# Kernel optimization log

Measured on AMD Instinct MI355X. Metric: run time of the kernel, lower is better.

## Reference

```python
import jax, jax.numpy as jnp
import numpy as np

B, LM, LX, D = 16, 1024, 1024, 768


def setup_inputs() -> dict:
    key = jax.random.key(0)
    k1, k2, k3, k4 = jax.random.split(key, 4)
    main = jax.random.normal(k1, (B, LM, D), dtype=jnp.float32)
    x = jax.random.normal(k2, (B, LX, D), dtype=jnp.float32)
    # keras 'uniform' init ~ U(-0.05, 0.05); scale to keep activations sane
    W = jax.random.uniform(k3, (D, D), dtype=jnp.float32, minval=-0.05, maxval=0.05)
    w = jax.random.uniform(k4, (2 * D, 1), dtype=jnp.float32, minval=-0.05, maxval=0.05)
    return {"main": main, "x": x, "W": W, "w": w}


def reference(main, x, W, w):
    # bilinear co-attention scores: (main @ W) . x^T -> (B, LM, LX)
    proj = jnp.einsum('bmd,de->bme', main, W)            # (B, LM, D)
    scores = jnp.einsum('bme,bne->bmn', proj, x)         # (B, LM, LX) -- no softmax in original
    A = jnp.einsum('bmn,bnd->bmd', scores, x)            # attended features (B, LM, D)
    s = main - A
    m = main * A
    outputs = jnp.concatenate([s, m], axis=-1)           # (B, LM, 2D)
    beta = jnp.einsum('bmk,k->bm', outputs, w[:, 0])     # (B, LM) -- raw, no softmax
    pooled = jnp.einsum('bm,bmk->bk', beta, outputs)     # weighted-sum pooling (B, 2D)
    return pooled
```

## Files before the change

kernel.cpp:

```cpp
#include <hip/hip_runtime.h>

constexpr int kB  = 16;
constexpr int kLM = 1024;
constexpr int kLX = 1024;
constexpr int kD  = 768;

using short8 = __attribute__((ext_vector_type(8))) short;
using f32x4  = __attribute__((ext_vector_type(4))) float;

__device__ __forceinline__ unsigned short f2bf(float f) {
    unsigned u = __float_as_uint(f);
    u = (u + 0x7FFF + ((u >> 16) & 1)) >> 16;
    return (unsigned short)u;
}
__device__ __forceinline__ float bf2f(unsigned short h) {
    return __uint_as_float(((unsigned)h) << 16);
}

__device__ __forceinline__ void gl_lds16(const unsigned short* g, unsigned short* l) {
    auto gp = (const __attribute__((address_space(1))) unsigned int*)g;
    auto lp = (__attribute__((address_space(3))) unsigned int*)l;
    __builtin_amdgcn_global_load_lds(gp, lp, 16, 0, 0);
}

__device__ __forceinline__ void writeChunk(unsigned short* dst, float4 lo, float4 hi) {
    union { short8 v; unsigned short u[8]; } o;
    o.u[0] = f2bf(lo.x); o.u[1] = f2bf(lo.y); o.u[2] = f2bf(lo.z); o.u[3] = f2bf(lo.w);
    o.u[4] = f2bf(hi.x); o.u[5] = f2bf(hi.y); o.u[6] = f2bf(hi.z); o.u[7] = f2bf(hi.w);
    *(short8*)dst = o.v;
}

__device__ __forceinline__ size_t chunk_off(int c, int K) {
    int sr = c >> 3, s = c & 7;
    int tt = s ^ (sr & 7);
    int r  = sr * 2 + (tt >> 2);
    int q  = tt & 3;
    return (size_t)r * K + q * 8;
}

__global__ __launch_bounds__(256) void transpose_cvt_kernel(
    const float* __restrict__ x, unsigned short* __restrict__ xT) {
    __shared__ float tile[64][65];
    const int b  = blockIdx.z;
    const int l0 = blockIdx.x * 64;
    const int d0 = blockIdx.y * 64;
    const int t  = threadIdx.x;
    const int tx = t & 15, ty = t >> 4;
    const float* xb = x + ((size_t)b * kLX + l0) * kD + d0;
#pragma unroll
    for (int p = 0; p < 4; ++p) {
        int r = p * 16 + ty;
        float4 v = *(const float4*)(xb + (size_t)r * kD + tx * 4);
        *(float4*)&tile[r][tx * 4] = v;
    }
    __syncthreads();
    unsigned short* xTb = xT + ((size_t)b * kD + d0) * kLX + l0;
#pragma unroll
    for (int p = 0; p < 4; ++p) {
        int dr = p * 16 + ty;
        ushort4 o;
        o.x = f2bf(tile[tx * 4 + 0][dr]);
        o.y = f2bf(tile[tx * 4 + 1][dr]);
        o.z = f2bf(tile[tx * 4 + 2][dr]);
        o.w = f2bf(tile[tx * 4 + 3][dr]);
        *(ushort4*)(xTb + (size_t)dr * kLX + tx * 4) = o;
    }
}

template <bool AFP32, bool BFP32>
__global__ __launch_bounds__(256) void gemm_nt_kernel(
    const void* __restrict__ Av, const void* __restrict__ Bv,
    unsigned short* __restrict__ C, int M, int N, int K,
    long sA, long sB, long sC) {
    __shared__ unsigned short Asm[2][128 * 32];
    __shared__ unsigned short Bsm[2][128 * 32];
    const int b  = blockIdx.z;
    const int i0 = blockIdx.x * 128;
    const int j0 = blockIdx.y * 128;
    const int t    = threadIdx.x;
    const int wave = t >> 6, lane = t & 63;
    const int wr = (wave >> 1) * 64, wc = (wave & 1) * 64;
    const int quad = lane >> 4, l15 = lane & 15;

    const unsigned short* Abh = AFP32 ? nullptr
        : (const unsigned short*)Av + (size_t)b * sA + (size_t)i0 * K;
    const unsigned short* Bbh = BFP32 ? nullptr
        : (const unsigned short*)Bv + (size_t)b * sB + (size_t)j0 * K;
    const float* Abf = AFP32
        ? (const float*)Av + (size_t)b * sA + (size_t)i0 * K : nullptr;
    const float* Bbf = BFP32
        ? (const float*)Bv + (size_t)b * sB + (size_t)j0 * K : nullptr;

    const int c0 = t, c1 = t + 256;
    const size_t off0 = chunk_off(c0, K);
    const size_t off1 = chunk_off(c1, K);

    const int sfr  = ((l15 & 1) * 4 + quad) ^ ((l15 >> 1) & 7);
    const int aOff = wr * 32 + (l15 >> 1) * 64 + sfr * 8;
    const int bOff = wc * 32 + (l15 >> 1) * 64 + sfr * 8;

    f32x4 acc[4][4];
    const f32x4 z = {0.f, 0.f, 0.f, 0.f};
#pragma unroll
    for (int i = 0; i < 4; ++i)
#pragma unroll
        for (int j = 0; j < 4; ++j) acc[i][j] = z;

    const int T = K >> 5;
    float4 pa0, pa1, pa2, pa3, pb0, pb1, pb2, pb3;

    if constexpr (AFP32) {
        writeChunk(Asm[0] + c0 * 8, *(const float4*)(Abf + off0),
                                    *(const float4*)(Abf + off0 + 4));
        writeChunk(Asm[0] + c1 * 8, *(const float4*)(Abf + off1),
                                    *(const float4*)(Abf + off1 + 4));
    } else {
        gl_lds16(Abh + off0, Asm[0] + c0 * 8);
        gl_lds16(Abh + off1, Asm[0] + c1 * 8);
    }
    if constexpr (BFP32) {
        writeChunk(Bsm[0] + c0 * 8, *(const float4*)(Bbf + off0),
                                    *(const float4*)(Bbf + off0 + 4));
        writeChunk(Bsm[0] + c1 * 8, *(const float4*)(Bbf + off1),
                                    *(const float4*)(Bbf + off1 + 4));
    } else {
        gl_lds16(Bbh + off0, Bsm[0] + c0 * 8);
        gl_lds16(Bbh + off1, Bsm[0] + c1 * 8);
    }
    if constexpr (AFP32) {
        pa0 = *(const float4*)(Abf + off0 + 32);
        pa1 = *(const float4*)(Abf + off0 + 36);
        pa2 = *(const float4*)(Abf + off1 + 32);
        pa3 = *(const float4*)(Abf + off1 + 36);
    }
    if constexpr (BFP32) {
        pb0 = *(const float4*)(Bbf + off0 + 32);
        pb1 = *(const float4*)(Bbf + off0 + 36);
        pb2 = *(const float4*)(Bbf + off1 + 32);
        pb3 = *(const float4*)(Bbf + off1 + 36);
    }

    int buf = 0;
    for (int kt = 0; kt < T; ++kt) {
        __syncthreads();
        if (kt + 1 < T) {
            const size_t k = (size_t)(kt + 1) << 5;
            if constexpr (AFP32) {
                writeChunk(Asm[buf ^ 1] + c0 * 8, pa0, pa1);
                writeChunk(Asm[buf ^ 1] + c1 * 8, pa2, pa3);
            } else {
                gl_lds16(Abh + off0 + k, Asm[buf ^ 1] + c0 * 8);
                gl_lds16(Abh + off1 + k, Asm[buf ^ 1] + c1 * 8);
            }
            if constexpr (BFP32) {
                writeChunk(Bsm[buf ^ 1] + c0 * 8, pb0, pb1);
                writeChunk(Bsm[buf ^ 1] + c1 * 8, pb2, pb3);
            } else {
                gl_lds16(Bbh + off0 + k, Bsm[buf ^ 1] + c0 * 8);
                gl_lds16(Bbh + off1 + k, Bsm[buf ^ 1] + c1 * 8);
            }
        }
        if (kt + 2 < T) {
            const size_t k2 = (size_t)(kt + 2) << 5;
            if constexpr (AFP32) {
                pa0 = *(const float4*)(Abf + off0 + k2);
                pa1 = *(const float4*)(Abf + off0 + k2 + 4);
                pa2 = *(const float4*)(Abf + off1 + k2);
                pa3 = *(const float4*)(Abf + off1 + k2 + 4);
            }
            if constexpr (BFP32) {
                pb0 = *(const float4*)(Bbf + off0 + k2);
                pb1 = *(const float4*)(Bbf + off0 + k2 + 4);
                pb2 = *(const float4*)(Bbf + off1 + k2);
                pb3 = *(const float4*)(Bbf + off1 + k2 + 4);
            }
        }
        const unsigned short* aP = Asm[buf] + aOff;
        const unsigned short* bP = Bsm[buf] + bOff;
        short8 af[4], bg[4];
#pragma unroll
        for (int i = 0; i < 4; ++i) af[i] = *(const short8*)(aP + i * 512);
#pragma unroll
        for (int j = 0; j < 4; ++j) bg[j] = *(const short8*)(bP + j * 512);
#pragma unroll
        for (int i = 0; i < 4; ++i)
#pragma unroll
            for (int j = 0; j < 4; ++j)
                acc[i][j] = __builtin_amdgcn_mfma_f32_16x16x32_bf16(
                    af[i], bg[j], acc[i][j], 0, 0, 0);
        buf ^= 1;
    }

    unsigned short* Cb = C + (size_t)b * sC + (size_t)(i0 + wr) * N + j0 + wc;
#pragma unroll
    for (int i = 0; i < 4; ++i)
#pragma unroll
        for (int j = 0; j < 4; ++j)
#pragma unroll
            for (int r = 0; r < 4; ++r)
                Cb[(size_t)(i * 16 + quad * 4 + r) * N + j * 16 + l15] =
                    f2bf(acc[i][j][r]);
}

__global__ __launch_bounds__(256) void pool_kernel(
    const float* __restrict__ mainp, const unsigned short* __restrict__ Aout,
    const float* __restrict__ w, float* __restrict__ out) {
    __shared__ float red[4][24][64];
    const int b     = blockIdx.y;
    const int chunk = blockIdx.x;
    const int t     = threadIdx.x;
    const int wave  = t >> 6, lane = t & 63;
    float w1[12], w2[12], ps[12], pm[12];
#pragma unroll
    for (int s = 0; s < 12; ++s) {
        w1[s] = w[s * 64 + lane];
        w2[s] = w[kD + s * 64 + lane];
        ps[s] = 0.f; pm[s] = 0.f;
    }
#pragma unroll
    for (int rr = 0; rr < 4; ++rr) {
        const int row = chunk * 16 + rr * 4 + wave;
        const float* mr = mainp + ((size_t)b * kLM + row) * kD;
        const unsigned short* ar = Aout + ((size_t)b * kLM + row) * kD;
        float sv[12], mv[12], acc = 0.f;
#pragma unroll
        for (int s = 0; s < 12; ++s) {
            float m_ = mr[s * 64 + lane];
            float a_ = bf2f(ar[s * 64 + lane]);
            sv[s] = m_ - a_;
            mv[s] = m_ * a_;
            acc += sv[s] * w1[s] + mv[s] * w2[s];
        }
#pragma unroll
        for (int off = 32; off; off >>= 1) acc += __shfl_xor(acc, off);
#pragma unroll
        for (int s = 0; s < 12; ++s) { ps[s] += acc * sv[s]; pm[s] += acc * mv[s]; }
    }
#pragma unroll
    for (int s = 0; s < 12; ++s) {
        red[wave][s][lane]      = ps[s];
        red[wave][12 + s][lane] = pm[s];
    }
    __syncthreads();
    float* ob = out + (size_t)b * 2 * kD;
    for (int v = t; v < 24 * 64; v += 256) {
        const int sl = v >> 6, ln = v & 63;
        const float sum = red[0][sl][ln] + red[1][sl][ln] +
                          red[2][sl][ln] + red[3][sl][ln];
        const int d = (sl < 12) ? sl * 64 + ln : kD + (sl - 12) * 64 + ln;
        atomicAdd(&ob[d], sum);
    }
}

extern "C" void kernel_launch(void* const* d_in, const int* in_sizes, int n_in,
                              void* d_out, int out_size, void* d_ws, size_t ws_size,
                              hipStream_t stream) {
    const float* mainp = (const float*)d_in[0];
    const float* x     = (const float*)d_in[1];
    const float* W     = (const float*)d_in[2];
    const float* w     = (const float*)d_in[3];
    float* out = (float*)d_out;

    char* p = (char*)d_ws;
    unsigned short* xT = (unsigned short*)p; p += (size_t)kB * kD * kLX * 2;
    unsigned short* G  = (unsigned short*)p; p += (size_t)kB * kD * kD * 2;
    unsigned short* Mt = (unsigned short*)p; p += (size_t)kB * kD * kD * 2;
    unsigned short* Ao = (unsigned short*)p; p += (size_t)kB * kLM * kD * 2;

    hipMemsetAsync(out, 0, (size_t)kB * 2 * kD * sizeof(float), stream);

    transpose_cvt_kernel<<<dim3(kLX / 64, kD / 64, kB), 256, 0, stream>>>(x, xT);

    gemm_nt_kernel<false, false><<<dim3(kD / 128, kD / 128, kB), 256, 0, stream>>>(
        xT, xT, G, kD, kD, kLX, (long)kD * kLX, (long)kD * kLX, (long)kD * kD);
    gemm_nt_kernel<false, true><<<dim3(kD / 128, kD / 128, kB), 256, 0, stream>>>(
        G, W, Mt, kD, kD, kD, (long)kD * kD, 0L, (long)kD * kD);
    gemm_nt_kernel<true, false><<<dim3(kLM / 128, kD / 128, kB), 256, 0, stream>>>(
        mainp, Mt, Ao, kLM, kD, kD, (long)kLM * kD, (long)kD * kD, (long)kLM * kD);

    pool_kernel<<<dim3(kLM / 16, kB), 256, 0, stream>>>(mainp, Ao, w, out);
}
```

Baseline: 244.3 us.

## Triple-buffer GEMM loads, exploit Gram symmetry, pre-convert inputs, remap blocks per XCD

Several changes go in together. The GEMM is reworked into a three-stage LDS pipeline that uses async global-to-LDS loads with explicit vmcnt waits and raised MFMA priority. For the symmetric x^T x Gram matrix, only the lower-triangle tiles are computed and each is mirrored by a transposed store. The fp32 inputs main and W are converted to bf16 up front by a separate kernel, replacing in-loop conversion. A 1D grid maps each batch to one XCD for L2 locality. The costs are an extra conversion pass over main, reuse of the xT buffer for mainBF, and more LDS per block.

New measurement: 230.3 us. 1.06x faster.

```diff
diff --git a/kernel.cpp b/kernel.cpp
--- a/kernel.cpp
+++ b/kernel.cpp
@@ -67,29 +67,51 @@
     }
 }
 
-template <bool AFP32, bool BFP32>
+__global__ __launch_bounds__(256) void cvt2_kernel(
+    const float* __restrict__ a, unsigned short* __restrict__ oa, int na8,
+    const float* __restrict__ b, unsigned short* __restrict__ ob, int nb8) {
+    int i = blockIdx.x * 256 + threadIdx.x;
+    const float* src;
+    unsigned short* dst;
+    if (i < na8) {
+        src = a + (size_t)i * 8; dst = oa + (size_t)i * 8;
+    } else {
+        int j = i - na8;
+        if (j >= nb8) return;
+        src = b + (size_t)j * 8; dst = ob + (size_t)j * 8;
+    }
+    float4 lo = *(const float4*)src;
+    float4 hi = *(const float4*)(src + 4);
+    writeChunk(dst, lo, hi);
+}
+
+template <bool SYMM>
 __global__ __launch_bounds__(256) void gemm_nt_kernel(
-    const void* __restrict__ Av, const void* __restrict__ Bv,
+    const unsigned short* __restrict__ A, const unsigned short* __restrict__ B,
     unsigned short* __restrict__ C, int M, int N, int K,
-    long sA, long sB, long sC) {
-    __shared__ unsigned short Asm[2][128 * 32];
-    __shared__ unsigned short Bsm[2][128 * 32];
-    const int b  = blockIdx.z;
-    const int i0 = blockIdx.x * 128;
-    const int j0 = blockIdx.y * 128;
+    long sA, long sB, long sC, int gx, int gy) {
+    __shared__ unsigned short Asm[3][128 * 32];
+    __shared__ unsigned short Bsm[3][128 * 32];
+
+    const int wgid = blockIdx.x;
+    const int xcd  = wgid & 7;
+    const int kk   = wgid >> 3;
+    const int tpb  = gx * gy;
+    const int grp  = kk / tpb;
+    const int til  = kk - grp * tpb;
+    const int b    = grp * 8 + xcd;
+    const int bi   = til % gx;
+    const int bj   = til / gx;
+    if (SYMM && bi < bj) return;
+    const int i0 = bi * 128, j0 = bj * 128;
+
     const int t    = threadIdx.x;
     const int wave = t >> 6, lane = t & 63;
     const int wr = (wave >> 1) * 64, wc = (wave & 1) * 64;
     const int quad = lane >> 4, l15 = lane & 15;
 
-    const unsigned short* Abh = AFP32 ? nullptr
-        : (const unsigned short*)Av + (size_t)b * sA + (size_t)i0 * K;
-    const unsigned short* Bbh = BFP32 ? nullptr
-        : (const unsigned short*)Bv + (size_t)b * sB + (size_t)j0 * K;
-    const float* Abf = AFP32
-        ? (const float*)Av + (size_t)b * sA + (size_t)i0 * K : nullptr;
-    const float* Bbf = BFP32
-        ? (const float*)Bv + (size_t)b * sB + (size_t)j0 * K : nullptr;
+    const unsigned short* Ab = A + (size_t)b * sA + (size_t)i0 * K;
+    const unsigned short* Bb = B + (size_t)b * sB + (size_t)j0 * K;
 
     const int c0 = t, c1 = t + 256;
     const size_t off0 = chunk_off(c0, K);
@@ -107,88 +129,54 @@
         for (int j = 0; j < 4; ++j) acc[i][j] = z;
 
     const int T = K >> 5;
-    float4 pa0, pa1, pa2, pa3, pb0, pb1, pb2, pb3;
-
-    if constexpr (AFP32) {
-        writeChunk(Asm[0] + c0 * 8, *(const float4*)(Abf + off0),
-                                    *(const float4*)(Abf + off0 + 4));
-        writeChunk(Asm[0] + c1 * 8, *(const float4*)(Abf + off1),
-                                    *(const float4*)(Abf + off1 + 4));
-    } else {
-        gl_lds16(Abh + off0, Asm[0] + c0 * 8);
-        gl_lds16(Abh + off1, Asm[0] + c1 * 8);
-    }
-    if constexpr (BFP32) {
-        writeChunk(Bsm[0] + c0 * 8, *(const float4*)(Bbf + off0),
-                                    *(const float4*)(Bbf + off0 + 4));
-        writeChunk(Bsm[0] + c1 * 8, *(const float4*)(Bbf + off1),
-                                    *(const float4*)(Bbf + off1 + 4));
-    } else {
-        gl_lds16(Bbh + off0, Bsm[0] + c0 * 8);
-        gl_lds16(Bbh + off1, Bsm[0] + c1 * 8);
-    }
-    if constexpr (AFP32) {
-        pa0 = *(const float4*)(Abf + off0 + 32);
-        pa1 = *(const float4*)(Abf + off0 + 36);
-        pa2 = *(const float4*)(Abf + off1 + 32);
-        pa3 = *(const float4*)(Abf + off1 + 36);
-    }
-    if constexpr (BFP32) {
-        pb0 = *(const float4*)(Bbf + off0 + 32);
-        pb1 = *(const float4*)(Bbf + off0 + 36);
-        pb2 = *(const float4*)(Bbf + off1 + 32);
-        pb3 = *(const float4*)(Bbf + off1 + 36);
-    }
-
-    int buf = 0;
+
+    gl_lds16(Ab + off0, Asm[0] + c0 * 8);
+    gl_lds16(Ab + off1, Asm[0] + c1 * 8);
+    gl_lds16(Bb + off0, Bsm[0] + c0 * 8);
+    gl_lds16(Bb + off1, Bsm[0] + c1 * 8);
+    if (T > 1) {
+        gl_lds16(Ab + off0 + 32, Asm[1] + c0 * 8);
+        gl_lds16(Ab + off1 + 32, Asm[1] + c1 * 8);
+        gl_lds16(Bb + off0 + 32, Bsm[1] + c0 * 8);
+        gl_lds16(Bb + off1 + 32, Bsm[1] + c1 * 8);
+    }
+
+    int cur = 0;
     for (int kt = 0; kt < T; ++kt) {
-        __syncthreads();
-        if (kt + 1 < T) {
-            const size_t k = (size_t)(kt + 1) << 5;
-            if constexpr (AFP32) {
-                writeChunk(Asm[buf ^ 1] + c0 * 8, pa0, pa1);
-                writeChunk(Asm[buf ^ 1] + c1 * 8, pa2, pa3);
-            } else {
-                gl_lds16(Abh + off0 + k, Asm[buf ^ 1] + c0 * 8);
-                gl_lds16(Abh + off1 + k, Asm[buf ^ 1] + c1 * 8);
-            }
-            if constexpr (BFP32) {
-                writeChunk(Bsm[buf ^ 1] + c0 * 8, pb0, pb1);
-                writeChunk(Bsm[buf ^ 1] + c1 * 8, pb2, pb3);
-            } else {
-                gl_lds16(Bbh + off0 + k, Bsm[buf ^ 1] + c0 * 8);
-                gl_lds16(Bbh + off1 + k, Bsm[buf ^ 1] + c1 * 8);
-            }
+        if (kt + 2 < T) {
+            int nb = cur + 2; if (nb >= 3) nb -= 3;
+            const size_t k = (size_t)(kt + 2) << 5;
+            gl_lds16(Ab + off0 + k, Asm[nb] + c0 * 8);
+            gl_lds16(Ab + off1 + k, Asm[nb] + c1 * 8);
+            gl_lds16(Bb + off0 + k, Bsm[nb] + c0 * 8);
+            gl_lds16(Bb + off1 + k, Bsm[nb] + c1 * 8);
+            asm volatile("s_waitcnt vmcnt(8)" ::: "memory");
+        } else if (kt + 1 < T) {
+            asm volatile("s_waitcnt vmcnt(4)" ::: "memory");
+        } else {
+            asm volatile("s_waitcnt vmcnt(0)" ::: "memory");
         }
-        if (kt + 2 < T) {
-            const size_t k2 = (size_t)(kt + 2) << 5;
-            if constexpr (AFP32) {
-                pa0 = *(const float4*)(Abf + off0 + k2);
-                pa1 = *(const float4*)(Abf + off0 + k2 + 4);
-                pa2 = *(const float4*)(Abf + off1 + k2);
-                pa3 = *(const float4*)(Abf + off1 + k2 + 4);
-            }
-            if constexpr (BFP32) {
-                pb0 = *(const float4*)(Bbf + off0 + k2);
-                pb1 = *(const float4*)(Bbf + off0 + k2 + 4);
-                pb2 = *(const float4*)(Bbf + off1 + k2);
-                pb3 = *(const float4*)(Bbf + off1 + k2 + 4);
-            }
-        }
-        const unsigned short* aP = Asm[buf] + aOff;
-        const unsigned short* bP = Bsm[buf] + bOff;
+        __builtin_amdgcn_s_barrier();
+        asm volatile("" ::: "memory");
+
+        const unsigned short* aP = Asm[cur] + aOff;
+        const unsigned short* bP = Bsm[cur] + bOff;
         short8 af[4], bg[4];
 #pragma unroll
         for (int i = 0; i < 4; ++i) af[i] = *(const short8*)(aP + i * 512);
 #pragma unroll
         for (int j = 0; j < 4; ++j) bg[j] = *(const short8*)(bP + j * 512);
+        __builtin_amdgcn_s_setprio(1);
 #pragma unroll
         for (int i = 0; i < 4; ++i)
 #pragma unroll
             for (int j = 0; j < 4; ++j)
                 acc[i][j] = __builtin_amdgcn_mfma_f32_16x16x32_bf16(
                     af[i], bg[j], acc[i][j], 0, 0, 0);
-        buf ^= 1;
+        __builtin_amdgcn_s_setprio(0);
+        asm volatile("" ::: "memory");
+        __builtin_amdgcn_s_barrier();
+        cur = cur + 1; if (cur == 3) cur = 0;
     }
 
     unsigned short* Cb = C + (size_t)b * sC + (size_t)(i0 + wr) * N + j0 + wc;
@@ -200,6 +188,21 @@
             for (int r = 0; r < 4; ++r)
                 Cb[(size_t)(i * 16 + quad * 4 + r) * N + j * 16 + l15] =
                     f2bf(acc[i][j][r]);
+
+    if (SYMM && bi > bj) {
+        unsigned short* Cm = C + (size_t)b * sC + (size_t)(j0 + wc) * N + i0 + wr;
+#pragma unroll
+        for (int i = 0; i < 4; ++i)
+#pragma unroll
+            for (int j = 0; j < 4; ++j) {
+                ushort4 o;
+                o.x = f2bf(acc[i][j][0]);
+                o.y = f2bf(acc[i][j][1]);
+                o.z = f2bf(acc[i][j][2]);
+                o.w = f2bf(acc[i][j][3]);
+                *(ushort4*)(Cm + (size_t)(j * 16 + l15) * N + i * 16 + quad * 4) = o;
+            }
+    }
 }
 
 __global__ __launch_bounds__(256) void pool_kernel(
@@ -262,21 +265,31 @@
     float* out = (float*)d_out;
 
     char* p = (char*)d_ws;
-    unsigned short* xT = (unsigned short*)p; p += (size_t)kB * kD * kLX * 2;
-    unsigned short* G  = (unsigned short*)p; p += (size_t)kB * kD * kD * 2;
-    unsigned short* Mt = (unsigned short*)p; p += (size_t)kB * kD * kD * 2;
-    unsigned short* Ao = (unsigned short*)p; p += (size_t)kB * kLM * kD * 2;
+    unsigned short* xT  = (unsigned short*)p; p += (size_t)kB * kD * kLX * 2;
+    unsigned short* G   = (unsigned short*)p; p += (size_t)kB * kD * kD * 2;
+    unsigned short* Mt  = (unsigned short*)p; p += (size_t)kB * kD * kD * 2;
+    unsigned short* Ao  = (unsigned short*)p; p += (size_t)kB * kLM * kD * 2;
+    unsigned short* Wbf = (unsigned short*)p; p += (size_t)kD * kD * 2;
+    unsigned short* mainBF = xT;
 
     hipMemsetAsync(out, 0, (size_t)kB * 2 * kD * sizeof(float), stream);
 
     transpose_cvt_kernel<<<dim3(kLX / 64, kD / 64, kB), 256, 0, stream>>>(x, xT);
 
-    gemm_nt_kernel<false, false><<<dim3(kD / 128, kD / 128, kB), 256, 0, stream>>>(
-        xT, xT, G, kD, kD, kLX, (long)kD * kLX, (long)kD * kLX, (long)kD * kD);
-    gemm_nt_kernel<false, true><<<dim3(kD / 128, kD / 128, kB), 256, 0, stream>>>(
-        G, W, Mt, kD, kD, kD, (long)kD * kD, 0L, (long)kD * kD);
-    gemm_nt_kernel<true, false><<<dim3(kLM / 128, kD / 128, kB), 256, 0, stream>>>(
-        mainp, Mt, Ao, kLM, kD, kD, (long)kLM * kD, (long)kD * kD, (long)kLM * kD);
+    gemm_nt_kernel<true><<<dim3(kB * 36), 256, 0, stream>>>(
+        xT, xT, G, kD, kD, kLX, (long)kD * kLX, (long)kD * kLX, (long)kD * kD,
+        6, 6);
+
+    cvt2_kernel<<<dim3((kB * kLM * kD / 8 + kD * kD / 8 + 255) / 256), 256, 0,
+                  stream>>>(mainp, mainBF, kB * kLM * kD / 8, W, Wbf,
+                            kD * kD / 8);
+
+    gemm_nt_kernel<false><<<dim3(kB * 36), 256, 0, stream>>>(
+        G, Wbf, Mt, kD, kD, kD, (long)kD * kD, 0L, (long)kD * kD, 6, 6);
+
+    gemm_nt_kernel<false><<<dim3(kB * 48), 256, 0, stream>>>(
+        mainBF, Mt, Ao, kLM, kD, kD, (long)kLM * kD, (long)kD * kD,
+        (long)kLM * kD, 8, 6);
 
     pool_kernel<<<dim3(kLM / 16, kB), 256, 0, stream>>>(mainp, Ao, w, out);
 }
```
